# Kernel optimization log

Measured on AMD Instinct MI355X. Metric: run time of the kernel, lower is better.

The kernel has to match this reference:

```python
import jax, jax.numpy as jnp
import numpy as np

N = 100000   # nodes
E = 1600000  # edges (avg degree 16)
D = 128      # hidden_sizes


def setup_inputs() -> dict:
    key = jax.random.key(0)
    ks = jax.random.split(key, 9)
    x = jax.random.normal(ks[0], (N, D), dtype=jnp.float32)
    edge_index = jax.random.randint(ks[1], (2, E), 0, N, dtype=jnp.int64)
    s = 1.0 / np.sqrt(D)
    Wl1 = jax.random.uniform(ks[2], (D, D), jnp.float32, -s, s)
    Wr1 = jax.random.uniform(ks[3], (D, D), jnp.float32, -s, s)
    b1 = jax.random.uniform(ks[4], (D,), jnp.float32, -s, s)
    Wl2 = jax.random.uniform(ks[5], (D, D), jnp.float32, -s, s)
    Wr2 = jax.random.uniform(ks[6], (D, D), jnp.float32, -s, s)
    b2 = jax.random.uniform(ks[7], (D,), jnp.float32, -s, s)
    return {"x": x, "edge_index": edge_index,
            "Wl1": Wl1, "Wr1": Wr1, "b1": b1,
            "Wl2": Wl2, "Wr2": Wr2, "b2": b2}


def _sage_conv(x, src, dst, Wl, Wr, b):
    # mean aggregation of source features onto destination nodes
    msg = x[src]                                              # [E, D] irregular gather
    agg = jax.ops.segment_sum(msg, dst, num_segments=N)       # [N, D] scatter-add
    deg = jax.ops.segment_sum(jnp.ones((src.shape[0],), x.dtype), dst,
                              num_segments=N)                 # [N]
    mean = agg / jnp.maximum(deg, 1.0)[:, None]
    # out = lin_l(mean_neighbors) + lin_r(x_self) + bias
    return mean @ Wl + x @ Wr + b


def reference(x, edge_index, Wl1, Wr1, b1, Wl2, Wr2, b2):
    src, dst = edge_index[0], edge_index[1]
    h = jax.nn.relu(_sage_conv(x, src, dst, Wl1, Wr1, b1))
    h = _sage_conv(h, src, dst, Wl2, Wr2, b2)
    # Dropout: eval mode -> identity
    return h
```

## Files before the change

kernel.cpp:

```cpp
#include <hip/hip_runtime.h>

#define NN 100000
#define NE 1600000
#define D  128
#define PAD 128

typedef short  s16x8 __attribute__((ext_vector_type(8)));
typedef float  f32x4 __attribute__((ext_vector_type(4)));
typedef unsigned short u16;
typedef unsigned int   u32;

__device__ __forceinline__ u16 f2bf_rn(float f) {
    u32 u = __float_as_uint(f);
    u += 0x7FFFu + ((u >> 16) & 1u);
    return (u16)(u >> 16);
}
__device__ __forceinline__ void split2(float f, u16& h, u16& l) {
    u16 hh = f2bf_rn(f);
    float hf = __uint_as_float(((u32)hh) << 16);
    h = hh;
    l = f2bf_rn(f - hf);
}
__device__ __forceinline__ float bf2f(u16 h) {
    return __uint_as_float(((u32)h) << 16);
}

__global__ __launch_bounds__(256) void prep_x(const float* __restrict__ x,
                                              u16* __restrict__ xh) {
    int t = blockIdx.x * blockDim.x + threadIdx.x;
    if (t >= NN * D / 4) return;
    float4 v = ((const float4*)x)[t];
    ushort4 h;
    h.x = f2bf_rn(v.x); h.y = f2bf_rn(v.y);
    h.z = f2bf_rn(v.z); h.w = f2bf_rn(v.w);
    ((ushort4*)xh)[t] = h;
}

__global__ __launch_bounds__(256) void prep_w(const float* __restrict__ Wl1,
                                              const float* __restrict__ Wr1,
                                              const float* __restrict__ Wl2,
                                              const float* __restrict__ Wr2,
                                              u16* __restrict__ wth, u16* __restrict__ wtl) {
    int t = blockIdx.x * blockDim.x + threadIdx.x;
    if (t >= 2 * D * 2 * D) return;
    int layer = t >> 15;
    int c = (t >> 8) & 127;
    int k = t & 255;
    const float* Wl = layer ? Wl2 : Wl1;
    const float* Wr = layer ? Wr2 : Wr1;
    float v = (k < D) ? Wl[k * D + c] : Wr[(k - D) * D + c];
    u16 h, l; split2(v, h, l);
    wth[t] = h; wtl[t] = l;
}

__global__ void fill_kernel(const int* __restrict__ src, const int* __restrict__ dst,
                            int* __restrict__ deg, int* __restrict__ srcs) {
    int i = blockIdx.x * blockDim.x + threadIdx.x;
    if (i < NE) {
        int d = dst[i];
        int p = atomicAdd(&deg[d], 1);
        srcs[(size_t)d * PAD + p] = src[i];
    }
}

__global__ __launch_bounds__(256) void agg_kernel(const u16* __restrict__ Fh,
                                                  const int* __restrict__ deg,
                                                  const int* __restrict__ srcs,
                                                  u16* __restrict__ mh) {
    int gid  = blockIdx.x * blockDim.x + threadIdx.x;
    int node = gid >> 6;
    if (node >= NN) return;
    int lane = threadIdx.x & 63;
    int half = lane >> 5;
    int li   = lane & 31;
    int cnt  = deg[node];
    const int* es = srcs + (size_t)node * PAD;
    const ushort4* Fp = (const ushort4*)Fh;
    float a0 = 0.f, a1 = 0.f, a2 = 0.f, a3 = 0.f;
    int e = 0;
    for (; e + 4 <= cnt; e += 4) {
        int s0 = es[e + half];
        int s1 = es[e + 2 + half];
        ushort4 v0 = Fp[(size_t)s0 * 32 + li];
        ushort4 v1 = Fp[(size_t)s1 * 32 + li];
        a0 += bf2f(v0.x) + bf2f(v1.x);
        a1 += bf2f(v0.y) + bf2f(v1.y);
        a2 += bf2f(v0.z) + bf2f(v1.z);
        a3 += bf2f(v0.w) + bf2f(v1.w);
    }
    if (e + 2 <= cnt) {
        int s0 = es[e + half];
        ushort4 v0 = Fp[(size_t)s0 * 32 + li];
        a0 += bf2f(v0.x); a1 += bf2f(v0.y);
        a2 += bf2f(v0.z); a3 += bf2f(v0.w);
        e += 2;
    }
    if (e < cnt && half == 0) {
        int s0 = es[e];
        ushort4 v0 = Fp[(size_t)s0 * 32 + li];
        a0 += bf2f(v0.x); a1 += bf2f(v0.y);
        a2 += bf2f(v0.z); a3 += bf2f(v0.w);
    }
    a0 += __shfl_xor(a0, 32, 64);
    a1 += __shfl_xor(a1, 32, 64);
    a2 += __shfl_xor(a2, 32, 64);
    a3 += __shfl_xor(a3, 32, 64);
    if (half == 0) {
        float sc = 1.0f / fmaxf((float)cnt, 1.0f);
        ushort4 h;
        h.x = f2bf_rn(a0 * sc); h.y = f2bf_rn(a1 * sc);
        h.z = f2bf_rn(a2 * sc); h.w = f2bf_rn(a3 * sc);
        ((ushort4*)mh)[(size_t)node * 32 + li] = h;
    }
}

__global__ __launch_bounds__(256) void gemm_mfma(
    const u16* __restrict__ Am, const u16* __restrict__ As,
    const u16* __restrict__ Wth, const u16* __restrict__ Wtl,
    const float* __restrict__ bias, float* __restrict__ out,
    u16* __restrict__ Hh, int relu, int writeH, int writeOut)
{
    const int tid  = threadIdx.x;
    const int wave = tid >> 6;
    const int lane = tid & 63;
    const int lr   = lane & 15;
    const int kg   = lane >> 4;
    const int wcol = wave * 32;
    const int row0 = blockIdx.x * 128;

    f32x4 acc[8][2] = {};

#pragma unroll
    for (int ks = 0; ks < 8; ++ks) {
        const u16* A = (ks < 4) ? Am : As;
        const int ko = (ks & 3) * 32 + kg * 8;
        const int kw = ks * 32 + kg * 8;

        s16x8 bh0 = *(const s16x8*)&Wth[(size_t)(wcol + lr) * 256 + kw];
        s16x8 bh1 = *(const s16x8*)&Wth[(size_t)(wcol + 16 + lr) * 256 + kw];
        s16x8 bl0 = *(const s16x8*)&Wtl[(size_t)(wcol + lr) * 256 + kw];
        s16x8 bl1 = *(const s16x8*)&Wtl[(size_t)(wcol + 16 + lr) * 256 + kw];

#pragma unroll
        for (int rf = 0; rf < 8; ++rf) {
            int ar = row0 + rf * 16 + lr;
            if (ar >= NN) ar = NN - 1;
            s16x8 a = *(const s16x8*)&A[(size_t)ar * D + ko];
            acc[rf][0] = __builtin_amdgcn_mfma_f32_16x16x32_bf16(a, bh0, acc[rf][0], 0, 0, 0);
            acc[rf][1] = __builtin_amdgcn_mfma_f32_16x16x32_bf16(a, bh1, acc[rf][1], 0, 0, 0);
            acc[rf][0] = __builtin_amdgcn_mfma_f32_16x16x32_bf16(a, bl0, acc[rf][0], 0, 0, 0);
            acc[rf][1] = __builtin_amdgcn_mfma_f32_16x16x32_bf16(a, bl1, acc[rf][1], 0, 0, 0);
        }
    }

    __syncthreads();

    float b0 = bias[wcol + lr];
    float b1 = bias[wcol + 16 + lr];
#pragma unroll
    for (int rf = 0; rf < 8; ++rf) {
#pragma unroll
        for (int j = 0; j < 4; ++j) {
            int row = row0 + rf * 16 + kg * 4 + j;
            if (row >= NN) continue;
            float v0 = acc[rf][0][j] + b0;
            float v1 = acc[rf][1][j] + b1;
            if (relu) { v0 = fmaxf(v0, 0.f); v1 = fmaxf(v1, 0.f); }
            if (writeOut) {
                out[(size_t)row * D + wcol + lr]      = v0;
                out[(size_t)row * D + wcol + 16 + lr] = v1;
            }
            if (writeH) {
                Hh[(size_t)row * D + wcol + lr]      = f2bf_rn(v0);
                Hh[(size_t)row * D + wcol + 16 + lr] = f2bf_rn(v1);
            }
        }
    }
}

extern "C" void kernel_launch(void* const* d_in, const int* in_sizes, int n_in,
                              void* d_out, int out_size, void* d_ws, size_t ws_size,
                              hipStream_t stream) {
    const float* x   = (const float*)d_in[0];
    const int*   ei  = (const int*)d_in[1];
    const float* Wl1 = (const float*)d_in[2];
    const float* Wr1 = (const float*)d_in[3];
    const float* b1  = (const float*)d_in[4];
    const float* Wl2 = (const float*)d_in[5];
    const float* Wr2 = (const float*)d_in[6];
    const float* b2  = (const float*)d_in[7];
    float* out = (float*)d_out;

    const int* srcE = ei;
    const int* dstE = ei + NE;

    u16* xh  = (u16*)d_ws;
    u16* mh  = xh + (size_t)NN * D;
    u16* wth = mh + (size_t)NN * D;
    u16* wtl = wth + 2 * D * 2 * D;
    int* deg  = (int*)(wtl + 2 * D * 2 * D);
    int* srcs = deg + NN;

    hipMemsetAsync(deg, 0, sizeof(int) * NN, stream);

    prep_x<<<(NN * D / 4 + 255) / 256, 256, 0, stream>>>(x, xh);
    prep_w<<<(2 * D * 2 * D + 255) / 256, 256, 0, stream>>>(Wl1, Wr1, Wl2, Wr2, wth, wtl);
    fill_kernel<<<(NE + 255) / 256, 256, 0, stream>>>(srcE, dstE, deg, srcs);

    const int aggGrid  = (NN * 64 + 255) / 256;
    const int gemmGrid = (NN + 127) / 128;

    agg_kernel<<<aggGrid, 256, 0, stream>>>(xh, deg, srcs, mh);
    gemm_mfma<<<gemmGrid, 256, 0, stream>>>(mh, xh, wth, wtl, b1, out,
                                            xh, 1, 1, 0);

    agg_kernel<<<aggGrid, 256, 0, stream>>>(xh, deg, srcs, mh);
    gemm_mfma<<<gemmGrid, 256, 0, stream>>>(mh, xh,
                                            wth + 2 * D * D, wtl + 2 * D * D, b2, out,
                                            (u16*)nullptr, 0, 0, 1);
}
```

Before: 485.1 us.

## Partition CSR fill by destination slice and widen aggregation gathers to 16B

The fill kernel becomes a grid-stride loop in which each block handles only destinations whose low three bits match its slice. This presumably aims to localise atomics and scattered writes per XCD, but every edge index is now read eight times. The per-node neighbor slot padding drops from 128 to 64, which halves the srcs buffer but overflows if any node has more than 64 in-edges. The aggregation kernel has each lane load 8 bf16 values (16 bytes) for one of four edges at a time, then reduces across the four lane groups with shuffles.

```diff
diff --git a/kernel.cpp b/kernel.cpp
--- a/kernel.cpp
+++ b/kernel.cpp
@@ -3,12 +3,13 @@
 #define NN 100000
 #define NE 1600000
 #define D  128
-#define PAD 128
+#define PAD 64
 
 typedef short  s16x8 __attribute__((ext_vector_type(8)));
 typedef float  f32x4 __attribute__((ext_vector_type(4)));
 typedef unsigned short u16;
 typedef unsigned int   u32;
+typedef u16 u16x8 __attribute__((ext_vector_type(8)));
 
 __device__ __forceinline__ u16 f2bf_rn(float f) {
     u32 u = __float_as_uint(f);
@@ -53,13 +54,19 @@
     wth[t] = h; wtl[t] = l;
 }
 
-__global__ void fill_kernel(const int* __restrict__ src, const int* __restrict__ dst,
-                            int* __restrict__ deg, int* __restrict__ srcs) {
-    int i = blockIdx.x * blockDim.x + threadIdx.x;
-    if (i < NE) {
+__global__ __launch_bounds__(256) void fill_kernel(const int* __restrict__ src,
+                                                   const int* __restrict__ dst,
+                                                   int* __restrict__ deg,
+                                                   int* __restrict__ srcs) {
+    int slice  = blockIdx.x & 7;
+    int group  = blockIdx.x >> 3;
+    int stride = (gridDim.x >> 3) * blockDim.x;
+    for (int i = group * blockDim.x + threadIdx.x; i < NE; i += stride) {
         int d = dst[i];
-        int p = atomicAdd(&deg[d], 1);
-        srcs[(size_t)d * PAD + p] = src[i];
+        if ((d & 7) == slice) {
+            int p = atomicAdd(&deg[d], 1);
+            srcs[(size_t)d * PAD + p] = src[i];
+        }
     }
 }
 
@@ -71,46 +78,39 @@
     int node = gid >> 6;
     if (node >= NN) return;
     int lane = threadIdx.x & 63;
-    int half = lane >> 5;
-    int li   = lane & 31;
+    int cg   = lane >> 4;
+    int cl   = lane & 15;
     int cnt  = deg[node];
     const int* es = srcs + (size_t)node * PAD;
-    const ushort4* Fp = (const ushort4*)Fh;
-    float a0 = 0.f, a1 = 0.f, a2 = 0.f, a3 = 0.f;
-    int e = 0;
-    for (; e + 4 <= cnt; e += 4) {
-        int s0 = es[e + half];
-        int s1 = es[e + 2 + half];
-        ushort4 v0 = Fp[(size_t)s0 * 32 + li];
-        ushort4 v1 = Fp[(size_t)s1 * 32 + li];
-        a0 += bf2f(v0.x) + bf2f(v1.x);
-        a1 += bf2f(v0.y) + bf2f(v1.y);
-        a2 += bf2f(v0.z) + bf2f(v1.z);
-        a3 += bf2f(v0.w) + bf2f(v1.w);
-    }
-    if (e + 2 <= cnt) {
-        int s0 = es[e + half];
-        ushort4 v0 = Fp[(size_t)s0 * 32 + li];
-        a0 += bf2f(v0.x); a1 += bf2f(v0.y);
-        a2 += bf2f(v0.z); a3 += bf2f(v0.w);
-        e += 2;
-    }
-    if (e < cnt && half == 0) {
-        int s0 = es[e];
-        ushort4 v0 = Fp[(size_t)s0 * 32 + li];
-        a0 += bf2f(v0.x); a1 += bf2f(v0.y);
-        a2 += bf2f(v0.z); a3 += bf2f(v0.w);
-    }
-    a0 += __shfl_xor(a0, 32, 64);
-    a1 += __shfl_xor(a1, 32, 64);
-    a2 += __shfl_xor(a2, 32, 64);
-    a3 += __shfl_xor(a3, 32, 64);
-    if (half == 0) {
+
+    float a[8] = {0.f, 0.f, 0.f, 0.f, 0.f, 0.f, 0.f, 0.f};
+    for (int e = 0; e < cnt; e += 8) {
+        int g0 = e + cg, g1 = e + 4 + cg;
+        bool t0 = g0 < cnt, t1 = g1 < cnt;
+        int s0 = es[t0 ? g0 : 0];
+        int s1 = es[t1 ? g1 : 0];
+        u16x8 v0 = *(const u16x8*)&Fh[(size_t)s0 * D + cl * 8];
+        u16x8 v1 = *(const u16x8*)&Fh[(size_t)s1 * D + cl * 8];
+        if (t0) {
+#pragma unroll
+            for (int j = 0; j < 8; ++j) a[j] += bf2f(v0[j]);
+        }
+        if (t1) {
+#pragma unroll
+            for (int j = 0; j < 8; ++j) a[j] += bf2f(v1[j]);
+        }
+    }
+#pragma unroll
+    for (int j = 0; j < 8; ++j) {
+        a[j] += __shfl_xor(a[j], 16, 64);
+        a[j] += __shfl_xor(a[j], 32, 64);
+    }
+    if (lane < 16) {
         float sc = 1.0f / fmaxf((float)cnt, 1.0f);
-        ushort4 h;
-        h.x = f2bf_rn(a0 * sc); h.y = f2bf_rn(a1 * sc);
-        h.z = f2bf_rn(a2 * sc); h.w = f2bf_rn(a3 * sc);
-        ((ushort4*)mh)[(size_t)node * 32 + li] = h;
+        u16x8 h;
+#pragma unroll
+        for (int j = 0; j < 8; ++j) h[j] = f2bf_rn(a[j] * sc);
+        *(u16x8*)&mh[(size_t)node * D + lane * 8] = h;
     }
 }
 
@@ -205,7 +205,7 @@
 
     prep_x<<<(NN * D / 4 + 255) / 256, 256, 0, stream>>>(x, xh);
     prep_w<<<(2 * D * 2 * D + 255) / 256, 256, 0, stream>>>(Wl1, Wr1, Wl2, Wr2, wth, wtl);
-    fill_kernel<<<(NE + 255) / 256, 256, 0, stream>>>(srcE, dstE, deg, srcs);
+    fill_kernel<<<2048, 256, 0, stream>>>(srcE, dstE, deg, srcs);
 
     const int aggGrid  = (NN * 64 + 255) / 256;
     const int gemmGrid = (NN + 127) / 128;
```

Result: faster. 432.6 us (-10.8%).
